# Kernel optimization log

Measured on AMD Instinct MI355X. Metric: run time of the kernel, lower is better.

The kernel has to match this reference:

```python
import jax, jax.numpy as jnp
import numpy as np


def _pick(key, nodes, mask, cnt):
    # Uniformly pick one of the `cnt` entries of `nodes` where mask is True.
    r = jax.random.randint(key, (), 0, jnp.maximum(cnt, 1))
    cs = jnp.cumsum(mask.astype(jnp.int32))
    return nodes[jnp.argmax(cs == r + 1)]


def _one_walk(key, nbrs, f0, n_faces, L):
    # nbrs: [N,3] int32 neighbor table, f0: scalar start face.
    seq = jnp.zeros((L + 1,), jnp.int32).at[0].set(f0)
    visited = jnp.zeros((n_faces + 1,), bool).at[n_faces].set(True).at[f0].set(True)

    def cond(st):
        return st[2] <= L

    def body(st):
        seq, visited, i, bs, k = st
        k, k1, k2, k3 = jax.random.split(k, 4)
        cur = seq[i - 1]
        nb = nbrs[cur]                     # [3] neighbor candidates
        unv = ~visited[nb]
        cnt = unv.sum()
        need = cnt == 0                    # stuck -> backtrack
        cand = _pick(k1, nb, unv, cnt)

        def bcond(c):
            bs_c, found = c[0], c[1]
            return need & (~found) & (i > bs_c)

        def bbody(c):
            bs_c, found, ta, kk = c
            kk, kp = jax.random.split(kk)
            back = seq[i - bs_c - 1]
            bn = nbrs[back]
            bm = ~visited[bn]
            bc = bm.sum()
            f2 = bc > 0
            ta2 = _pick(kp, bn, bm, bc)
            return (jnp.where(f2, bs_c, bs_c + 2), f2, jnp.where(f2, ta2, ta), kk)

        bs_f, found, ta_bt, _ = jax.lax.while_loop(
            bcond, bbody, (bs, jnp.array(False), jnp.int32(0), k2))
        rand_node = jax.random.randint(k3, (), 0, n_faces, dtype=jnp.int32)
        to_add = jnp.where(~need, cand, jnp.where(found, ta_bt, rand_node))
        hit = need & found                 # successful backtrack
        bs_new = jnp.where(hit, bs_f, jnp.int32(1))
        i_new = jnp.where(hit, i - bs_f, i)
        ar = jnp.arange(L + 1, dtype=jnp.int32)
        # torch: replace seq[i-bs:i] with to_add on successful backtrack
        seq = jnp.where(hit & (ar >= i_new) & (ar < i), to_add, seq)
        visited = visited.at[to_add].set(True)
        seq = seq.at[i_new].set(to_add)
        return (seq, visited, i_new + 1, bs_new, k)

    seq, *_ = jax.lax.while_loop(
        cond, body, (seq, visited, jnp.int32(1), jnp.int32(1), key))
    return seq


def patch_random_walk(key, neighbors, centers, n_faces, seq_len):
    B, G = centers.shape
    keys = jax.random.split(key, B * G).reshape(B, G)
    walk_g = jax.vmap(_one_walk, in_axes=(0, None, 0, None, None))
    walk_bg = jax.vmap(walk_g, in_axes=(0, 0, 0, None, None))
    return walk_bg(keys, neighbors, centers, n_faces, seq_len)  # [B,G,L+1] int32


def setup_inputs() -> dict:
    key = jax.random.key(0)
    k1, k2, k3 = jax.random.split(key, 3)
    B, N, G = 4, 20000, 1024
    xyz = jax.random.normal(k1, (B, N, 3), dtype=jnp.float32)
    neighbors = jax.random.randint(k2, (B, N, 3), 0, N, dtype=jnp.int32)
    centers = jax.random.randint(k3, (B, G), 0, N, dtype=jnp.int32)
    return {"xyz": xyz, "neighbors": neighbors, "centers": centers,
            "n_faces": N, "seq_len": 63}


def reference(xyz, neighbors, centers, n_faces, seq_len):
    # patch_random_walk -> idx [B,G,K]; then Group.forward gather + recenter.
    idx = patch_random_walk(jax.random.key(42), neighbors, centers, n_faces, seq_len)
    gather = jax.vmap(lambda p, i: p[i])(xyz, idx)            # [B,G,K,3]
    center_xyz = jax.vmap(lambda p, c: p[c])(xyz, centers)    # [B,G,3]
    return gather - center_xyz[:, :, None, :]
```

## Files before the change

kernel.cpp:

```cpp
#include <hip/hip_runtime.h>
#include <stdint.h>
#include <stddef.h>


namespace {

__device__ __forceinline__ uint32_t rotl32(uint32_t x, int r) {
  return (x << r) | (x >> (32 - r));
}

__device__ __forceinline__ void tf2x32(uint32_t ka, uint32_t kb,
                                       uint32_t x0, uint32_t x1,
                                       uint32_t& o0, uint32_t& o1) {
  const uint32_t kc = ka ^ kb ^ 0x1BD11BDAu;
  x0 += ka; x1 += kb;
#define TF_R4(r0, r1, r2, r3)                          \
  x0 += x1; x1 = rotl32(x1, r0); x1 ^= x0;             \
  x0 += x1; x1 = rotl32(x1, r1); x1 ^= x0;             \
  x0 += x1; x1 = rotl32(x1, r2); x1 ^= x0;             \
  x0 += x1; x1 = rotl32(x1, r3); x1 ^= x0;
  TF_R4(13, 15, 26, 6)  x0 += kb; x1 += kc + 1u;
  TF_R4(17, 29, 16, 24) x0 += kc; x1 += ka + 2u;
  TF_R4(13, 15, 26, 6)  x0 += ka; x1 += kb + 3u;
  TF_R4(17, 29, 16, 24) x0 += kb; x1 += kc + 4u;
  TF_R4(13, 15, 26, 6)  x0 += kc; x1 += ka + 5u;
#undef TF_R4
  o0 = x0; o1 = x1;
}

__device__ __forceinline__ void randbits(uint32_t ka, uint32_t kb,
                                         uint32_t& hi, uint32_t& lo) {
  uint32_t s0a, s0b, s1a, s1b, h0, h1;
  tf2x32(ka, kb, 0u, 0u, s0a, s0b);
  tf2x32(ka, kb, 0u, 1u, s1a, s1b);
  tf2x32(s0a, s0b, 0u, 0u, h0, h1);
  hi = h0 ^ h1;
  tf2x32(s1a, s1b, 0u, 0u, h0, h1);
  lo = h0 ^ h1;
}

__device__ __forceinline__ uint32_t r_generic(uint32_t hi, uint32_t lo,
                                              uint32_t span) {
  uint32_t mult = 65536u % span;
  mult = (mult * mult) % span;
  return ((hi % span) * mult + (lo % span)) % span;
}

__device__ __forceinline__ uint32_t pick_code(uint32_t hi, uint32_t lo) {
  return ((hi % 3u + lo % 3u) % 3u) | ((lo & 1u) << 2);
}

constexpr int WPB = 16;
constexpr int CH = 64;
constexpr int NMAX = 20352;
constexpr int VISW = 636;

__global__ __launch_bounds__(1024) void walk_kernel(
    const float* __restrict__ xyz, const int* __restrict__ nbrs,
    const int* __restrict__ centers, const int* __restrict__ n_faces_p,
    const int* __restrict__ seq_len_p, float* __restrict__ out,
    int s0, int num_walks, int Lp1) {
  __shared__ uint32_t nb01L[NMAX];
  __shared__ uint16_t nb2L[NMAX];
  __shared__ uint32_t visL[WPB * VISW];

  const int tid = threadIdx.x;
  const int wv = tid >> 6, lane = tid & 63;
  const int w0 = blockIdx.x * WPB;
  if (w0 >= num_walks) return;
  const int w = w0 + wv;
  const bool active = (w < num_walks);

  const int N = *n_faces_p;
  const int L = *seq_len_p;
  const int B = s0 / (3 * N);
  const int G = num_walks / B;
  const bool lds_ok = (N <= NMAX) && (G % WPB == 0);

  const int bb = (active ? w : w0) / G;
  const int* __restrict__ nb   = nbrs + (size_t)bb * N * 3;
  const float* __restrict__ xb = xyz + (size_t)bb * N * 3;

  const int f0 = active ? centers[w] : 0;
  int3 grow = make_int3(0, 0, 0);
  if (!lds_ok && active)
    grow = *reinterpret_cast<const int3*>(nb + 3 * (size_t)f0);

  if (wv == 0) {
    if (lane < WPB && (w0 + lane) < num_walks) {
      uint32_t ka, kb;
      tf2x32(0u, 42u, 0u, (uint32_t)(w0 + lane), ka, kb);
      visL[(lane * CH + 0) * 2 + 0] = ka;
      visL[(lane * CH + 0) * 2 + 1] = kb;
#pragma clang loop unroll(disable)
      for (int c2 = 1; c2 < CH; ++c2) {
        tf2x32(ka, kb, 0u, 0u, ka, kb);
        visL[(lane * CH + c2) * 2 + 0] = ka;
        visL[(lane * CH + c2) * 2 + 1] = kb;
      }
    }
  } else if (lds_ok) {
    for (int r = tid - 64; r < N; r += 960) {
      const int3 v = *reinterpret_cast<const int3*>(nb + 3 * (size_t)r);
      nb01L[r] = (uint32_t)v.x | ((uint32_t)v.y << 16);
      nb2L[r]  = (uint16_t)v.z;
    }
  }
  __syncthreads();

  const uint32_t mka = visL[(wv * CH + lane) * 2 + 0];
  const uint32_t mkb = visL[(wv * CH + lane) * 2 + 1];
  uint32_t mycode;
  {
    uint32_t k1a, k1b, hi, lo;
    tf2x32(mka, mkb, 0u, 1u, k1a, k1b);
    randbits(k1a, k1b, hi, lo);
    mycode = pick_code(hi, lo);
  }
  __syncthreads();

  if (!active) return;

  uint32_t extka = 0, extkb = 0;
  int extc = -1;
  auto get_key = [&](int idx, uint32_t& ra, uint32_t& rb) {
    if (idx < CH) {
      ra = (uint32_t)__shfl((int)mka, idx);
      rb = (uint32_t)__shfl((int)mkb, idx);
    } else {
      if (extc < 0) {
        extka = (uint32_t)__shfl((int)mka, CH - 1);
        extkb = (uint32_t)__shfl((int)mkb, CH - 1);
        extc = CH - 1;
      }
      while (extc < idx) { tf2x32(extka, extkb, 0u, 0u, extka, extkb); ++extc; }
      ra = extka; rb = extkb;
    }
  };

  int seqr = (lane == 0) ? f0 : -1;
  uint32_t code_next = (uint32_t)__shfl((int)mycode, 0);
  int i = 1, bs = 1, c = 0;

  if (lds_ok) {
    uint32_t* __restrict__ visW = visL + wv * VISW;
    for (int j = lane; j < VISW; j += 64) visW[j] = 0u;
    if (lane == 0) visW[(unsigned)f0 >> 5] = 1u << (f0 & 31);

    uint32_t p0 = nb01L[f0];
    int n0 = (int)(p0 & 0xffffu), n1 = (int)(p0 >> 16), n2 = (int)nb2L[f0];

    while (i <= L) {
      const int idx = c; ++c;
      const uint32_t pA = nb01L[n0]; const uint32_t a2 = nb2L[n0];
      const uint32_t pB = nb01L[n1]; const uint32_t b2 = nb2L[n1];
      const uint32_t pC = nb01L[n2]; const uint32_t c2v = nb2L[n2];
      const uint32_t wv0 = visW[(unsigned)n0 >> 5];
      const uint32_t wv1 = visW[(unsigned)n1 >> 5];
      const uint32_t wv2 = visW[(unsigned)n2 >> 5];
      const uint32_t codeP = code_next;
      code_next = (uint32_t)__shfl((int)mycode, (c < CH) ? c : 0);

      const uint32_t u0 = ((wv0 >> (n0 & 31)) & 1u) ^ 1u;
      const uint32_t u1 = ((wv1 >> (n1 & 31)) & 1u) ^ 1u;
      const uint32_t u2 = ((wv2 >> (n2 & 31)) & 1u) ^ 1u;
      const uint32_t cnt = u0 + u1 + u2;

      int to_add, sel;
      if (__builtin_expect(cnt == 0, 0)) {
        sel = -1;
        uint32_t kia, kib;
        get_key(idx, kia, kib);
        uint32_t kka, kkb;
        tf2x32(kia, kib, 0u, 2u, kka, kkb);
        bool found = false;
        int ta = 0, bsc = bs;
        while (!found && i > bsc) {
          uint32_t ca, cb, kpa, kpb;
          tf2x32(kka, kkb, 0u, 0u, ca, cb);
          tf2x32(kka, kkb, 0u, 1u, kpa, kpb);
          const int back = __shfl(seqr, i - bsc - 1);
          const uint32_t pm = nb01L[back];
          const int m0 = (int)(pm & 0xffffu), m1 = (int)(pm >> 16);
          const int m2 = (int)nb2L[back];
          const uint32_t e0 = ((visW[(unsigned)m0 >> 5] >> (m0 & 31)) & 1u) ^ 1u;
          const uint32_t e1 = ((visW[(unsigned)m1 >> 5] >> (m1 & 31)) & 1u) ^ 1u;
          const uint32_t e2 = ((visW[(unsigned)m2 >> 5] >> (m2 & 31)) & 1u) ^ 1u;
          const uint32_t bc = e0 + e1 + e2;
          if (bc > 0) {
            uint32_t bhi, blo;
            randbits(kpa, kpb, bhi, blo);
            const uint32_t bcode = pick_code(bhi, blo);
            const uint32_t r3 = bcode & 3u, r2 = (bcode >> 2) & 1u;
            const uint32_t t2v = (bc == 3 ? r3 : (bc == 2 ? r2 : 0)) + 1;
            ta = (e0 == t2v) ? m0 : ((e0 + e1 == t2v) ? m1 : m2);
            found = true;
          } else {
            bsc += 2;
          }
          kka = ca; kkb = cb;
        }
        if (found) {
          to_add = ta;
          const int i_new = i - bsc;
          seqr = (lane >= i_new && lane < i) ? to_add : seqr;
          bs = bsc; i = i_new;
        } else {
          uint32_t k3a, k3b, rhi, rlo;
          tf2x32(kia, kib, 0u, 3u, k3a, k3b);
          randbits(k3a, k3b, rhi, rlo);
          to_add = (int)r_generic(rhi, rlo, (uint32_t)N);
          bs = 1;
        }
        if (lane == 0)
          visW[(unsigned)to_add >> 5] |= 1u << (to_add & 31);
        seqr = (lane == i) ? to_add : seqr;
        ++i;
        const uint32_t p = nb01L[to_add];
        n0 = (int)(p & 0xffffu); n1 = (int)(p >> 16); n2 = (int)nb2L[to_add];
        continue;
      }
      uint32_t code = codeP;
      if (__builtin_expect(idx >= CH, 0)) {
        uint32_t ia, ib, k1a, k1b, hi, lo;
        get_key(idx, ia, ib);
        tf2x32(ia, ib, 0u, 1u, k1a, k1b);
        randbits(k1a, k1b, hi, lo);
        code = pick_code(hi, lo);
      }
      const uint32_t r3 = code & 3u, r2 = (code >> 2) & 1u;
      const uint32_t target = (cnt == 3 ? r3 : (cnt == 2 ? r2 : 0)) + 1;
      sel = (u0 == target) ? 0 : ((u0 + u1 == target) ? 1 : 2);
      to_add = (sel == 0) ? n0 : ((sel == 1) ? n1 : n2);
      const uint32_t wsel = (sel == 0) ? wv0 : ((sel == 1) ? wv1 : wv2);
      if (lane == 0)
        visW[(unsigned)to_add >> 5] = wsel | (1u << (to_add & 31));
      seqr = (lane == i) ? to_add : seqr;
      bs = 1; ++i;
      if (sel == 0)      { n0 = (int)(pA & 0xffffu); n1 = (int)(pA >> 16); n2 = (int)a2; }
      else if (sel == 1) { n0 = (int)(pB & 0xffffu); n1 = (int)(pB >> 16); n2 = (int)b2; }
      else               { n0 = (int)(pC & 0xffffu); n1 = (int)(pC >> 16); n2 = (int)c2v; }
    }
  } else {
    int hist  = (lane == 0) ? f0 : -1;
    int hist2 = -1;
    int3 row = grow;
    while (i <= L) {
      const int idx = c; ++c;
      const bool deep = (idx >= CH);
      const uint32_t codeP = code_next;
      code_next = (uint32_t)__shfl((int)mycode, (c < CH) ? c : 0);

      const int n0 = row.x, n1 = row.y, n2 = row.z;
      int v0 = __any(hist == n0), v1 = __any(hist == n1), v2 = __any(hist == n2);
      if (deep) {
        v0 |= __any(hist2 == n0); v1 |= __any(hist2 == n1); v2 |= __any(hist2 == n2);
      }
      const int u0 = 1 - v0, u1 = 1 - v1, u2 = 1 - v2;
      const int cnt = u0 + u1 + u2;

      int to_add;
      bool hit = false;
      int bsf = bs;
      if (cnt > 0) {
        uint32_t code = codeP;
        if (deep) {
          uint32_t ia, ib, k1a, k1b, hi, lo;
          get_key(idx, ia, ib);
          tf2x32(ia, ib, 0u, 1u, k1a, k1b);
          randbits(k1a, k1b, hi, lo);
          code = pick_code(hi, lo);
        }
        const int r3 = (int)(code & 3u), r2 = (int)((code >> 2) & 1u);
        const int target = (cnt == 3 ? r3 : (cnt == 2 ? r2 : 0)) + 1;
        to_add = (u0 == target) ? n0 : ((u0 + u1 == target) ? n1 : n2);
      } else {
        uint32_t kia, kib;
        get_key(idx, kia, kib);
        uint32_t kka, kkb;
        tf2x32(kia, kib, 0u, 2u, kka, kkb);
        bool found = false;
        int ta = 0, bsc = bs;
        while (!found && i > bsc) {
          uint32_t ca, cb, kpa, kpb;
          tf2x32(kka, kkb, 0u, 0u, ca, cb);
          tf2x32(kka, kkb, 0u, 1u, kpa, kpb);
          const int back = __shfl(seqr, i - bsc - 1);
          const int3 br = *reinterpret_cast<const int3*>(nb + 3 * (size_t)back);
          int w0m = __any(hist == br.x), w1m = __any(hist == br.y), w2m = __any(hist == br.z);
          if (deep) {
            w0m |= __any(hist2 == br.x); w1m |= __any(hist2 == br.y); w2m |= __any(hist2 == br.z);
          }
          const int e0 = 1 - w0m, e1 = 1 - w1m, e2 = 1 - w2m;
          const int bc = e0 + e1 + e2;
          if (bc > 0) {
            uint32_t bhi, blo;
            randbits(kpa, kpb, bhi, blo);
            const uint32_t bcode = pick_code(bhi, blo);
            const int r3 = (int)(bcode & 3u), r2 = (int)((bcode >> 2) & 1u);
            const int t2v = (bc == 3 ? r3 : (bc == 2 ? r2 : 0)) + 1;
            ta = (e0 == t2v) ? br.x : ((e0 + e1 == t2v) ? br.y : br.z);
            found = true;
          } else {
            bsc += 2;
          }
          kka = ca; kkb = cb;
        }
        if (found) {
          to_add = ta; hit = true; bsf = bsc;
        } else {
          uint32_t k3a, k3b, rhi, rlo;
          tf2x32(kia, kib, 0u, 3u, k3a, k3b);
          randbits(k3a, k3b, rhi, rlo);
          to_add = (int)r_generic(rhi, rlo, (uint32_t)N);
        }
      }

      int i_new, up;
      if (hit) { i_new = i - bsf; bs = bsf; up = i - 1; }
      else     { i_new = i;       bs = 1;   up = i; }
      seqr = (lane >= i_new && lane <= up) ? to_add : seqr;

      const int slot = idx + 1;
      if (slot < CH)          hist  = (lane == slot)      ? to_add : hist;
      else if (slot < 2 * CH) hist2 = (lane == slot - CH) ? to_add : hist2;

      i = i_new + 1;
      row = *reinterpret_cast<const int3*>(nb + 3 * (size_t)to_add);
    }
  }

  const float cx = xb[3 * (size_t)f0 + 0];
  const float cy = xb[3 * (size_t)f0 + 1];
  const float cz = xb[3 * (size_t)f0 + 2];
  if (lane < Lp1) {
    const int node = seqr;
    float3 v;
    v.x = xb[3 * (size_t)node + 0] - cx;
    v.y = xb[3 * (size_t)node + 1] - cy;
    v.z = xb[3 * (size_t)node + 2] - cz;
    *reinterpret_cast<float3*>(out + ((size_t)w * Lp1 + lane) * 3) = v;
  }
}

}

extern "C" void kernel_launch(void* const* d_in, const int* in_sizes, int n_in,
                              void* d_out, int out_size, void* d_ws, size_t ws_size,
                              hipStream_t stream) {
  const float* xyz     = (const float*)d_in[0];
  const int*   nbrs    = (const int*)d_in[1];
  const int*   centers = (const int*)d_in[2];
  const int*   n_faces = (const int*)d_in[3];
  const int*   seq_len = (const int*)d_in[4];
  float* out = (float*)d_out;

  const int s0 = in_sizes[0];
  const int num_walks = in_sizes[2];
  const int Lp1 = out_size / (3 * num_walks);

  const int blocks = (num_walks + WPB - 1) / WPB;
  walk_kernel<<<blocks, WPB * 64, 0, stream>>>(
      xyz, nbrs, centers, n_faces, seq_len, out, s0, num_walks, Lp1);
}
```

Measured before the change: 99.40 us.

## Pack two walks per wavefront using half-wave lanes, halve block size

Each 64-lane wavefront now runs two independent walks, one per 32-lane half, with sequence state split across two registers per lane and shuffles indexed within the half. The block shrinks from 16 to 8 waves while still handling 16 walks, so the per-block LDS neighbor table is shared by fewer threads. The LDS staging loop uses fewer loader waves. Divergence between the two packed walks forces backtrack paths to execute in lockstep under __any, which may add serialized work.

```diff
diff --git a/kernel.cpp b/kernel.cpp
--- a/kernel.cpp
+++ b/kernel.cpp
@@ -50,12 +50,13 @@
   return ((hi % 3u + lo % 3u) % 3u) | ((lo & 1u) << 2);
 }
 
+constexpr int WAVES = 8;
 constexpr int WPB = 16;
 constexpr int CH = 64;
 constexpr int NMAX = 20352;
 constexpr int VISW = 636;
 
-__global__ __launch_bounds__(1024) void walk_kernel(
+__global__ __launch_bounds__(512) void walk_kernel(
     const float* __restrict__ xyz, const int* __restrict__ nbrs,
     const int* __restrict__ centers, const int* __restrict__ n_faces_p,
     const int* __restrict__ seq_len_p, float* __restrict__ out,
@@ -66,25 +67,16 @@
 
   const int tid = threadIdx.x;
   const int wv = tid >> 6, lane = tid & 63;
+  const int hl = lane & 31;
+  const int hb = lane & 32;
   const int w0 = blockIdx.x * WPB;
   if (w0 >= num_walks) return;
-  const int w = w0 + wv;
-  const bool active = (w < num_walks);
 
   const int N = *n_faces_p;
   const int L = *seq_len_p;
   const int B = s0 / (3 * N);
   const int G = num_walks / B;
   const bool lds_ok = (N <= NMAX) && (G % WPB == 0);
-
-  const int bb = (active ? w : w0) / G;
-  const int* __restrict__ nb   = nbrs + (size_t)bb * N * 3;
-  const float* __restrict__ xb = xyz + (size_t)bb * N * 3;
-
-  const int f0 = active ? centers[w] : 0;
-  int3 grow = make_int3(0, 0, 0);
-  if (!lds_ok && active)
-    grow = *reinterpret_cast<const int3*>(nb + 3 * (size_t)f0);
 
   if (wv == 0) {
     if (lane < WPB && (w0 + lane) < num_walks) {
@@ -100,57 +92,74 @@
       }
     }
   } else if (lds_ok) {
-    for (int r = tid - 64; r < N; r += 960) {
-      const int3 v = *reinterpret_cast<const int3*>(nb + 3 * (size_t)r);
+    const int bb0 = w0 / G;
+    const int* __restrict__ nbT = nbrs + (size_t)bb0 * N * 3;
+    for (int r = tid - 64; r < N; r += (WAVES - 1) * 64) {
+      const int3 v = *reinterpret_cast<const int3*>(nbT + 3 * (size_t)r);
       nb01L[r] = (uint32_t)v.x | ((uint32_t)v.y << 16);
       nb2L[r]  = (uint16_t)v.z;
     }
   }
   __syncthreads();
 
-  const uint32_t mka = visL[(wv * CH + lane) * 2 + 0];
-  const uint32_t mkb = visL[(wv * CH + lane) * 2 + 1];
-  uint32_t mycode;
-  {
-    uint32_t k1a, k1b, hi, lo;
-    tf2x32(mka, mkb, 0u, 1u, k1a, k1b);
-    randbits(k1a, k1b, hi, lo);
-    mycode = pick_code(hi, lo);
-  }
-  __syncthreads();
-
-  if (!active) return;
-
-  uint32_t extka = 0, extkb = 0;
-  int extc = -1;
-  auto get_key = [&](int idx, uint32_t& ra, uint32_t& rb) {
-    if (idx < CH) {
-      ra = (uint32_t)__shfl((int)mka, idx);
-      rb = (uint32_t)__shfl((int)mkb, idx);
-    } else {
-      if (extc < 0) {
-        extka = (uint32_t)__shfl((int)mka, CH - 1);
-        extkb = (uint32_t)__shfl((int)mkb, CH - 1);
-        extc = CH - 1;
-      }
-      while (extc < idx) { tf2x32(extka, extkb, 0u, 0u, extka, extkb); ++extc; }
-      ra = extka; rb = extkb;
-    }
-  };
-
-  int seqr = (lane == 0) ? f0 : -1;
-  uint32_t code_next = (uint32_t)__shfl((int)mycode, 0);
-  int i = 1, bs = 1, c = 0;
-
   if (lds_ok) {
-    uint32_t* __restrict__ visW = visL + wv * VISW;
-    for (int j = lane; j < VISW; j += 64) visW[j] = 0u;
-    if (lane == 0) visW[(unsigned)f0 >> 5] = 1u << (f0 & 31);
+    const int kw = 2 * wv + (hb >> 5);
+    const int w = w0 + kw;
+    const bool act0 = (w < num_walks);
+    const int bb = (act0 ? w : w0) / G;
+    const float* __restrict__ xb = xyz + (size_t)bb * N * 3;
+    const int f0 = act0 ? centers[w] : 0;
+
+    const uint32_t mka0 = visL[(kw * CH + hl) * 2 + 0];
+    const uint32_t mkb0 = visL[(kw * CH + hl) * 2 + 1];
+    const uint32_t mka1 = visL[(kw * CH + hl + 32) * 2 + 0];
+    const uint32_t mkb1 = visL[(kw * CH + hl + 32) * 2 + 1];
+    uint32_t mycode0, mycode1;
+    {
+      uint32_t k1a, k1b, hi, lo;
+      tf2x32(mka0, mkb0, 0u, 1u, k1a, k1b);
+      randbits(k1a, k1b, hi, lo);
+      mycode0 = pick_code(hi, lo);
+      tf2x32(mka1, mkb1, 0u, 1u, k1a, k1b);
+      randbits(k1a, k1b, hi, lo);
+      mycode1 = pick_code(hi, lo);
+    }
+    __syncthreads();
+
+    uint32_t extka = 0, extkb = 0;
+    int extc = -1;
+    auto get_key = [&](int idxk, uint32_t& ra, uint32_t& rb) {
+      if (idxk < CH) {
+        const int sidx = (idxk & 31) | hb;
+        const uint32_t sa = (idxk < 32) ? mka0 : mka1;
+        const uint32_t sb = (idxk < 32) ? mkb0 : mkb1;
+        ra = (uint32_t)__shfl((int)sa, sidx);
+        rb = (uint32_t)__shfl((int)sb, sidx);
+      } else {
+        if (extc < 0) {
+          extka = (uint32_t)__shfl((int)mka1, 31 | hb);
+          extkb = (uint32_t)__shfl((int)mkb1, 31 | hb);
+          extc = CH - 1;
+        }
+        while (extc < idxk) { tf2x32(extka, extkb, 0u, 0u, extka, extkb); ++extc; }
+        ra = extka; rb = extkb;
+      }
+    };
+
+    uint32_t* __restrict__ visW = visL + kw * VISW;
+    for (int j = hl; j < VISW; j += 32) visW[j] = 0u;
+    if (hl == 0) visW[(unsigned)f0 >> 5] = 1u << (f0 & 31);
 
     uint32_t p0 = nb01L[f0];
     int n0 = (int)(p0 & 0xffffu), n1 = (int)(p0 >> 16), n2 = (int)nb2L[f0];
-
-    while (i <= L) {
+    int seqr0 = (hl == 0) ? f0 : -1;
+    int seqr1 = -1;
+    uint32_t code_next = (uint32_t)__shfl((int)mycode0, hb);
+    int i = act0 ? 1 : (L + 1);
+    int bs = 1, c = 0;
+
+    while (__any(i <= L)) {
+      const bool act = (i <= L);
       const int idx = c; ++c;
       const uint32_t pA = nb01L[n0]; const uint32_t a2 = nb2L[n0];
       const uint32_t pB = nb01L[n1]; const uint32_t b2 = nb2L[n1];
@@ -159,65 +168,94 @@
       const uint32_t wv1 = visW[(unsigned)n1 >> 5];
       const uint32_t wv2 = visW[(unsigned)n2 >> 5];
       const uint32_t codeP = code_next;
-      code_next = (uint32_t)__shfl((int)mycode, (c < CH) ? c : 0);
+      {
+        const int cc = (c < CH) ? c : 0;
+        const uint32_t csrc = (cc < 32) ? mycode0 : mycode1;
+        code_next = (uint32_t)__shfl((int)csrc, (cc & 31) | hb);
+      }
 
       const uint32_t u0 = ((wv0 >> (n0 & 31)) & 1u) ^ 1u;
       const uint32_t u1 = ((wv1 >> (n1 & 31)) & 1u) ^ 1u;
       const uint32_t u2 = ((wv2 >> (n2 & 31)) & 1u) ^ 1u;
       const uint32_t cnt = u0 + u1 + u2;
-
-      int to_add, sel;
-      if (__builtin_expect(cnt == 0, 0)) {
-        sel = -1;
+      const bool need = act && (cnt == 0);
+
+      if (__builtin_expect(__any(need), 0)) {
         uint32_t kia, kib;
         get_key(idx, kia, kib);
-        uint32_t kka, kkb;
-        tf2x32(kia, kib, 0u, 2u, kka, kkb);
+        uint32_t code = codeP;
+        if (idx >= CH) {
+          uint32_t k1a, k1b, hi, lo;
+          tf2x32(kia, kib, 0u, 1u, k1a, k1b);
+          randbits(k1a, k1b, hi, lo);
+          code = pick_code(hi, lo);
+        }
+        const uint32_t r3c = code & 3u, r2c = (code >> 2) & 1u;
+        const uint32_t tgt = (cnt == 3 ? r3c : (cnt == 2 ? r2c : 0)) + 1;
+        const int selc = (u0 == tgt) ? 0 : ((u0 + u1 == tgt) ? 1 : 2);
+        const int to_add_c = (selc == 0) ? n0 : ((selc == 1) ? n1 : n2);
+
         bool found = false;
         int ta = 0, bsc = bs;
-        while (!found && i > bsc) {
-          uint32_t ca, cb, kpa, kpb;
-          tf2x32(kka, kkb, 0u, 0u, ca, cb);
-          tf2x32(kka, kkb, 0u, 1u, kpa, kpb);
-          const int back = __shfl(seqr, i - bsc - 1);
-          const uint32_t pm = nb01L[back];
-          const int m0 = (int)(pm & 0xffffu), m1 = (int)(pm >> 16);
-          const int m2 = (int)nb2L[back];
-          const uint32_t e0 = ((visW[(unsigned)m0 >> 5] >> (m0 & 31)) & 1u) ^ 1u;
-          const uint32_t e1 = ((visW[(unsigned)m1 >> 5] >> (m1 & 31)) & 1u) ^ 1u;
-          const uint32_t e2 = ((visW[(unsigned)m2 >> 5] >> (m2 & 31)) & 1u) ^ 1u;
-          const uint32_t bc = e0 + e1 + e2;
-          if (bc > 0) {
-            uint32_t bhi, blo;
-            randbits(kpa, kpb, bhi, blo);
-            const uint32_t bcode = pick_code(bhi, blo);
-            const uint32_t r3 = bcode & 3u, r2 = (bcode >> 2) & 1u;
-            const uint32_t t2v = (bc == 3 ? r3 : (bc == 2 ? r2 : 0)) + 1;
-            ta = (e0 == t2v) ? m0 : ((e0 + e1 == t2v) ? m1 : m2);
-            found = true;
-          } else {
-            bsc += 2;
+        if (need) {
+          uint32_t kka, kkb;
+          tf2x32(kia, kib, 0u, 2u, kka, kkb);
+          while (!found && i > bsc) {
+            uint32_t ca, cb, kpa, kpb;
+            tf2x32(kka, kkb, 0u, 0u, ca, cb);
+            tf2x32(kka, kkb, 0u, 1u, kpa, kpb);
+            const int j = i - bsc - 1;
+            const int sidx = (j & 31) | hb;
+            const int bk0 = __shfl(seqr0, sidx);
+            const int bk1 = __shfl(seqr1, sidx);
+            const int back = (j < 32) ? bk0 : bk1;
+            const uint32_t pm = nb01L[back];
+            const int m0 = (int)(pm & 0xffffu), m1 = (int)(pm >> 16);
+            const int m2 = (int)nb2L[back];
+            const uint32_t e0 = ((visW[(unsigned)m0 >> 5] >> (m0 & 31)) & 1u) ^ 1u;
+            const uint32_t e1 = ((visW[(unsigned)m1 >> 5] >> (m1 & 31)) & 1u) ^ 1u;
+            const uint32_t e2 = ((visW[(unsigned)m2 >> 5] >> (m2 & 31)) & 1u) ^ 1u;
+            const uint32_t bc = e0 + e1 + e2;
+            if (bc > 0) {
+              uint32_t bhi, blo;
+              randbits(kpa, kpb, bhi, blo);
+              const uint32_t bcode = pick_code(bhi, blo);
+              const uint32_t br3 = bcode & 3u, br2 = (bcode >> 2) & 1u;
+              const uint32_t t2v = (bc == 3 ? br3 : (bc == 2 ? br2 : 0)) + 1;
+              ta = (e0 == t2v) ? m0 : ((e0 + e1 == t2v) ? m1 : m2);
+              found = true;
+            } else {
+              bsc += 2;
+            }
+            kka = ca; kkb = cb;
           }
-          kka = ca; kkb = cb;
-        }
-        if (found) {
-          to_add = ta;
-          const int i_new = i - bsc;
-          seqr = (lane >= i_new && lane < i) ? to_add : seqr;
-          bs = bsc; i = i_new;
-        } else {
+        }
+        int rnd = 0;
+        if (need && !found) {
           uint32_t k3a, k3b, rhi, rlo;
           tf2x32(kia, kib, 0u, 3u, k3a, k3b);
           randbits(k3a, k3b, rhi, rlo);
-          to_add = (int)r_generic(rhi, rlo, (uint32_t)N);
-          bs = 1;
-        }
-        if (lane == 0)
-          visW[(unsigned)to_add >> 5] |= 1u << (to_add & 31);
-        seqr = (lane == i) ? to_add : seqr;
-        ++i;
-        const uint32_t p = nb01L[to_add];
-        n0 = (int)(p & 0xffffu); n1 = (int)(p >> 16); n2 = (int)nb2L[to_add];
+          rnd = (int)r_generic(rhi, rlo, (uint32_t)N);
+        }
+        const bool hit = need && found;
+        const int to_add = need ? (found ? ta : rnd) : to_add_c;
+        const int i_new = hit ? (i - bsc) : i;
+        seqr0 = (hit && hl >= i_new && hl < i) ? to_add : seqr0;
+        seqr1 = (hit && (hl + 32) >= i_new && (hl + 32) < i) ? to_add : seqr1;
+        bs = act ? (hit ? bsc : 1) : bs;
+        i = i_new;
+        if (act && hl == 0) {
+          const uint32_t wd = visW[(unsigned)to_add >> 5];
+          visW[(unsigned)to_add >> 5] = wd | (1u << (to_add & 31));
+        }
+        seqr0 = (act && hl == i) ? to_add : seqr0;
+        seqr1 = (act && (hl + 32) == i) ? to_add : seqr1;
+        if (act) ++i;
+        const int sf = act ? to_add : 0;
+        const uint32_t p = nb01L[sf];
+        if (act) {
+          n0 = (int)(p & 0xffffu); n1 = (int)(p >> 16); n2 = (int)nb2L[sf];
+        }
         continue;
       }
       uint32_t code = codeP;
@@ -230,116 +268,176 @@
       }
       const uint32_t r3 = code & 3u, r2 = (code >> 2) & 1u;
       const uint32_t target = (cnt == 3 ? r3 : (cnt == 2 ? r2 : 0)) + 1;
-      sel = (u0 == target) ? 0 : ((u0 + u1 == target) ? 1 : 2);
-      to_add = (sel == 0) ? n0 : ((sel == 1) ? n1 : n2);
+      const int sel = (u0 == target) ? 0 : ((u0 + u1 == target) ? 1 : 2);
+      const int to_add = (sel == 0) ? n0 : ((sel == 1) ? n1 : n2);
       const uint32_t wsel = (sel == 0) ? wv0 : ((sel == 1) ? wv1 : wv2);
-      if (lane == 0)
+      if (act && hl == 0)
         visW[(unsigned)to_add >> 5] = wsel | (1u << (to_add & 31));
-      seqr = (lane == i) ? to_add : seqr;
-      bs = 1; ++i;
+      seqr0 = (act && hl == i) ? to_add : seqr0;
+      seqr1 = (act && (hl + 32) == i) ? to_add : seqr1;
+      if (act) { bs = 1; ++i; }
       if (sel == 0)      { n0 = (int)(pA & 0xffffu); n1 = (int)(pA >> 16); n2 = (int)a2; }
       else if (sel == 1) { n0 = (int)(pB & 0xffffu); n1 = (int)(pB >> 16); n2 = (int)b2; }
       else               { n0 = (int)(pC & 0xffffu); n1 = (int)(pC >> 16); n2 = (int)c2v; }
     }
+
+    if (act0) {
+      const float cx = xb[3 * (size_t)f0 + 0];
+      const float cy = xb[3 * (size_t)f0 + 1];
+      const float cz = xb[3 * (size_t)f0 + 2];
+      if (hl < Lp1) {
+        const int node = seqr0;
+        float3 v;
+        v.x = xb[3 * (size_t)node + 0] - cx;
+        v.y = xb[3 * (size_t)node + 1] - cy;
+        v.z = xb[3 * (size_t)node + 2] - cz;
+        *reinterpret_cast<float3*>(out + ((size_t)w * Lp1 + hl) * 3) = v;
+      }
+      if (hl + 32 < Lp1) {
+        const int node = seqr1;
+        float3 v;
+        v.x = xb[3 * (size_t)node + 0] - cx;
+        v.y = xb[3 * (size_t)node + 1] - cy;
+        v.z = xb[3 * (size_t)node + 2] - cz;
+        *reinterpret_cast<float3*>(out + ((size_t)w * Lp1 + hl + 32) * 3) = v;
+      }
+    }
   } else {
-    int hist  = (lane == 0) ? f0 : -1;
-    int hist2 = -1;
-    int3 row = grow;
-    while (i <= L) {
-      const int idx = c; ++c;
-      const bool deep = (idx >= CH);
-      const uint32_t codeP = code_next;
-      code_next = (uint32_t)__shfl((int)mycode, (c < CH) ? c : 0);
-
-      const int n0 = row.x, n1 = row.y, n2 = row.z;
-      int v0 = __any(hist == n0), v1 = __any(hist == n1), v2 = __any(hist == n2);
-      if (deep) {
-        v0 |= __any(hist2 == n0); v1 |= __any(hist2 == n1); v2 |= __any(hist2 == n2);
-      }
-      const int u0 = 1 - v0, u1 = 1 - v1, u2 = 1 - v2;
-      const int cnt = u0 + u1 + u2;
-
-      int to_add;
-      bool hit = false;
-      int bsf = bs;
-      if (cnt > 0) {
-        uint32_t code = codeP;
+    for (int sub = 0; sub < 2; ++sub) {
+      const int w = w0 + 2 * wv + sub;
+      if (w >= num_walks) continue;
+      const int bb = w / G;
+      const int* __restrict__ nbG = nbrs + (size_t)bb * N * 3;
+      const float* __restrict__ xb = xyz + (size_t)bb * N * 3;
+      const int f0 = centers[w];
+      const uint32_t mka = visL[((2 * wv + sub) * CH + lane) * 2 + 0];
+      const uint32_t mkb = visL[((2 * wv + sub) * CH + lane) * 2 + 1];
+      uint32_t mycode;
+      {
+        uint32_t k1a, k1b, hi, lo;
+        tf2x32(mka, mkb, 0u, 1u, k1a, k1b);
+        randbits(k1a, k1b, hi, lo);
+        mycode = pick_code(hi, lo);
+      }
+      uint32_t extka = 0, extkb = 0;
+      int extc = -1;
+      auto get_key = [&](int idxk, uint32_t& ra, uint32_t& rb) {
+        if (idxk < CH) {
+          ra = (uint32_t)__shfl((int)mka, idxk);
+          rb = (uint32_t)__shfl((int)mkb, idxk);
+        } else {
+          if (extc < 0) {
+            extka = (uint32_t)__shfl((int)mka, CH - 1);
+            extkb = (uint32_t)__shfl((int)mkb, CH - 1);
+            extc = CH - 1;
+          }
+          while (extc < idxk) { tf2x32(extka, extkb, 0u, 0u, extka, extkb); ++extc; }
+          ra = extka; rb = extkb;
+        }
+      };
+
+      int seqr = (lane == 0) ? f0 : -1;
+      uint32_t code_next = (uint32_t)__shfl((int)mycode, 0);
+      int i = 1, bs = 1, c = 0;
+      int hist  = (lane == 0) ? f0 : -1;
+      int hist2 = -1;
+      int3 row = *reinterpret_cast<const int3*>(nbG + 3 * (size_t)f0);
+      while (i <= L) {
+        const int idx = c; ++c;
+        const bool deep = (idx >= CH);
+        const uint32_t codeP = code_next;
+        code_next = (uint32_t)__shfl((int)mycode, (c < CH) ? c : 0);
+
+        const int n0 = row.x, n1 = row.y, n2 = row.z;
+        int v0 = __any(hist == n0), v1 = __any(hist == n1), v2 = __any(hist == n2);
         if (deep) {
-          uint32_t ia, ib, k1a, k1b, hi, lo;
-          get_key(idx, ia, ib);
-          tf2x32(ia, ib, 0u, 1u, k1a, k1b);
-          randbits(k1a, k1b, hi, lo);
-          code = pick_code(hi, lo);
-        }
-        const int r3 = (int)(code & 3u), r2 = (int)((code >> 2) & 1u);
-        const int target = (cnt == 3 ? r3 : (cnt == 2 ? r2 : 0)) + 1;
-        to_add = (u0 == target) ? n0 : ((u0 + u1 == target) ? n1 : n2);
-      } else {
-        uint32_t kia, kib;
-        get_key(idx, kia, kib);
-        uint32_t kka, kkb;
-        tf2x32(kia, kib, 0u, 2u, kka, kkb);
-        bool found = false;
-        int ta = 0, bsc = bs;
-        while (!found && i > bsc) {
-          uint32_t ca, cb, kpa, kpb;
-          tf2x32(kka, kkb, 0u, 0u, ca, cb);
-          tf2x32(kka, kkb, 0u, 1u, kpa, kpb);
-          const int back = __shfl(seqr, i - bsc - 1);
-          const int3 br = *reinterpret_cast<const int3*>(nb + 3 * (size_t)back);
-          int w0m = __any(hist == br.x), w1m = __any(hist == br.y), w2m = __any(hist == br.z);
+          v0 |= __any(hist2 == n0); v1 |= __any(hist2 == n1); v2 |= __any(hist2 == n2);
+        }
+        const int u0 = 1 - v0, u1 = 1 - v1, u2 = 1 - v2;
+        const int cnt = u0 + u1 + u2;
+
+        int to_add;
+        bool hit = false;
+        int bsf = bs;
+        if (cnt > 0) {
+          uint32_t code = codeP;
           if (deep) {
-            w0m |= __any(hist2 == br.x); w1m |= __any(hist2 == br.y); w2m |= __any(hist2 == br.z);
+            uint32_t ia, ib, k1a, k1b, hi, lo;
+            get_key(idx, ia, ib);
+            tf2x32(ia, ib, 0u, 1u, k1a, k1b);
+            randbits(k1a, k1b, hi, lo);
+            code = pick_code(hi, lo);
           }
-          const int e0 = 1 - w0m, e1 = 1 - w1m, e2 = 1 - w2m;
-          const int bc = e0 + e1 + e2;
-          if (bc > 0) {
-            uint32_t bhi, blo;
-            randbits(kpa, kpb, bhi, blo);
-            const uint32_t bcode = pick_code(bhi, blo);
-            const int r3 = (int)(bcode & 3u), r2 = (int)((bcode >> 2) & 1u);
-            const int t2v = (bc == 3 ? r3 : (bc == 2 ? r2 : 0)) + 1;
-            ta = (e0 == t2v) ? br.x : ((e0 + e1 == t2v) ? br.y : br.z);
-            found = true;
+          const int r3 = (int)(code & 3u), r2 = (int)((code >> 2) & 1u);
+          const int target = (cnt == 3 ? r3 : (cnt == 2 ? r2 : 0)) + 1;
+          to_add = (u0 == target) ? n0 : ((u0 + u1 == target) ? n1 : n2);
+        } else {
+          uint32_t kia, kib;
+          get_key(idx, kia, kib);
+          uint32_t kka, kkb;
+          tf2x32(kia, kib, 0u, 2u, kka, kkb);
+          bool found = false;
+          int ta = 0, bsc = bs;
+          while (!found && i > bsc) {
+            uint32_t ca, cb, kpa, kpb;
+            tf2x32(kka, kkb, 0u, 0u, ca, cb);
+            tf2x32(kka, kkb, 0u, 1u, kpa, kpb);
+            const int back = __shfl(seqr, i - bsc - 1);
+            const int3 br = *reinterpret_cast<const int3*>(nbG + 3 * (size_t)back);
+            int w0m = __any(hist == br.x), w1m = __any(hist == br.y), w2m = __any(hist == br.z);
+            if (deep) {
+              w0m |= __any(hist2 == br.x); w1m |= __any(hist2 == br.y); w2m |= __any(hist2 == br.z);
+            }
+            const int e0 = 1 - w0m, e1 = 1 - w1m, e2 = 1 - w2m;
+            const int bc = e0 + e1 + e2;
+            if (bc > 0) {
+              uint32_t bhi, blo;
+              randbits(kpa, kpb, bhi, blo);
+              const uint32_t bcode = pick_code(bhi, blo);
+              const int r3 = (int)(bcode & 3u), r2 = (int)((bcode >> 2) & 1u);
+              const int t2v = (bc == 3 ? r3 : (bc == 2 ? r2 : 0)) + 1;
+              ta = (e0 == t2v) ? br.x : ((e0 + e1 == t2v) ? br.y : br.z);
+              found = true;
+            } else {
+              bsc += 2;
+            }
+            kka = ca; kkb = cb;
+          }
+          if (found) {
+            to_add = ta; hit = true; bsf = bsc;
           } else {
-            bsc += 2;
+            uint32_t k3a, k3b, rhi, rlo;
+            tf2x32(kia, kib, 0u, 3u, k3a, k3b);
+            randbits(k3a, k3b, rhi, rlo);
+            to_add = (int)r_generic(rhi, rlo, (uint32_t)N);
           }
-          kka = ca; kkb = cb;
-        }
-        if (found) {
-          to_add = ta; hit = true; bsf = bsc;
-        } else {
-          uint32_t k3a, k3b, rhi, rlo;
-          tf2x32(kia, kib, 0u, 3u, k3a, k3b);
-          randbits(k3a, k3b, rhi, rlo);
-          to_add = (int)r_generic(rhi, rlo, (uint32_t)N);
-        }
-      }
-
-      int i_new, up;
-      if (hit) { i_new = i - bsf; bs = bsf; up = i - 1; }
-      else     { i_new = i;       bs = 1;   up = i; }
-      seqr = (lane >= i_new && lane <= up) ? to_add : seqr;
-
-      const int slot = idx + 1;
-      if (slot < CH)          hist  = (lane == slot)      ? to_add : hist;
-      else if (slot < 2 * CH) hist2 = (lane == slot - CH) ? to_add : hist2;
-
-      i = i_new + 1;
-      row = *reinterpret_cast<const int3*>(nb + 3 * (size_t)to_add);
-    }
-  }
-
-  const float cx = xb[3 * (size_t)f0 + 0];
-  const float cy = xb[3 * (size_t)f0 + 1];
-  const float cz = xb[3 * (size_t)f0 + 2];
-  if (lane < Lp1) {
-    const int node = seqr;
-    float3 v;
-    v.x = xb[3 * (size_t)node + 0] - cx;
-    v.y = xb[3 * (size_t)node + 1] - cy;
-    v.z = xb[3 * (size_t)node + 2] - cz;
-    *reinterpret_cast<float3*>(out + ((size_t)w * Lp1 + lane) * 3) = v;
+        }
+
+        int i_new, up;
+        if (hit) { i_new = i - bsf; bs = bsf; up = i - 1; }
+        else     { i_new = i;       bs = 1;   up = i; }
+        seqr = (lane >= i_new && lane <= up) ? to_add : seqr;
+
+        const int slot = idx + 1;
+        if (slot < CH)          hist  = (lane == slot)      ? to_add : hist;
+        else if (slot < 2 * CH) hist2 = (lane == slot - CH) ? to_add : hist2;
+
+        i = i_new + 1;
+        row = *reinterpret_cast<const int3*>(nbG + 3 * (size_t)to_add);
+      }
+
+      const float cx = xb[3 * (size_t)f0 + 0];
+      const float cy = xb[3 * (size_t)f0 + 1];
+      const float cz = xb[3 * (size_t)f0 + 2];
+      if (lane < Lp1) {
+        const int node = seqr;
+        float3 v;
+        v.x = xb[3 * (size_t)node + 0] - cx;
+        v.y = xb[3 * (size_t)node + 1] - cy;
+        v.z = xb[3 * (size_t)node + 2] - cz;
+        *reinterpret_cast<float3*>(out + ((size_t)w * Lp1 + lane) * 3) = v;
+      }
+    }
   }
 }
 
@@ -360,6 +458,6 @@
   const int Lp1 = out_size / (3 * num_walks);
 
   const int blocks = (num_walks + WPB - 1) / WPB;
-  walk_kernel<<<blocks, WPB * 64, 0, stream>>>(
+  walk_kernel<<<blocks, WAVES * 64, 0, stream>>>(
       xyz, nbrs, centers, n_faces, seq_len, out, s0, num_walks, Lp1);
 }
```

New measurement: 99.32 us. About the same (-0.1%).
